# Performance work log

Measured on AMD Instinct MI355X. Metric: run time of the kernel, lower is better.

## Reference

```python
import jax, jax.numpy as jnp
import numpy as np

GAMMA = 5e-4
IN_DIM, HID = 512, 4096
N = HID  # batch must equal hidden_dim for classifier(gram) to type-check


def setup_inputs() -> dict:
    key = jax.random.key(0)
    ks = jax.random.split(key, 7)
    s = lambda fan_in: 1.0 / np.sqrt(fan_in)
    return {
        "x": jax.random.normal(ks[0], (N, IN_DIM), jnp.float32),
        "W1": jax.random.uniform(ks[1], (HID, IN_DIM), jnp.float32, -s(IN_DIM), s(IN_DIM)),
        "b1": jax.random.uniform(ks[2], (HID,), jnp.float32, -s(IN_DIM), s(IN_DIM)),
        "W2": jax.random.uniform(ks[3], (HID, HID), jnp.float32, -s(HID), s(HID)),
        "b2": jax.random.uniform(ks[4], (HID,), jnp.float32, -s(HID), s(HID)),
        "Wc": jax.random.uniform(ks[5], (1, HID), jnp.float32, -s(HID), s(HID)),
        "bc": jax.random.uniform(ks[6], (1,), jnp.float32, -s(HID), s(HID)),
    }


def reference(x, W1, b1, W2, b2, Wc, bc):
    h = jnp.tanh(x @ W1.T + b1)          # [N, HID]
    h = jnp.tanh(h @ W2.T + b2)          # [N, HID]
    # KernelLayer: support = h.detach() (first call), RBF gram via cdist+exp
    support = jax.lax.stop_gradient(h)   # [N, HID]
    sq = (jnp.sum(h * h, axis=1, keepdims=True)
          + jnp.sum(support * support, axis=1)[None, :]
          - 2.0 * (h @ support.T))       # [N, N] squared distances
    gram = jnp.exp(-GAMMA * sq)
    return gram @ Wc.T + bc              # [N, 1]
```

## Files before the change

### kernel.cpp

```cpp
#include <hip/hip_runtime.h>
#include <hip/hip_bf16.h>


#define NROWS 4096
#define HID   4096
#define INDIM 512
#define GAMMA_F 5e-4f

typedef float f32x4  __attribute__((ext_vector_type(4)));
typedef int   i32x4  __attribute__((ext_vector_type(4)));
typedef int   i32x8  __attribute__((ext_vector_type(8)));

#define BAR() asm volatile("s_barrier" ::: "memory")
#define SCALE1 0x7F7F7F7F

__device__ __forceinline__ unsigned short f2bf_rne(float f) {
  union { float f; unsigned int u; } v; v.f = f;
  unsigned int r = v.u + 0x7FFFu + ((v.u >> 16) & 1u);
  return (unsigned short)(r >> 16);
}

__device__ __forceinline__ unsigned char f2e4m3(float x) {
  unsigned int u = __float_as_uint(x);
  unsigned char s = (unsigned char)((u >> 24) & 0x80u);
  float a = fabsf(x);
  if (a >= 448.f) return s | 0x7E;
  if (a < 0.015625f) {
    int q = (int)rintf(a * 512.f);
    return s | (unsigned char)q;
  }
  unsigned int ua = u & 0x7fffffffu;
  ua += 0x7FFFFu + ((ua >> 20) & 1u);
  int e = (int)(ua >> 23) - 127;
  unsigned int m = (ua >> 20) & 7u;
  return s | (unsigned char)(((e + 7) << 3) | m);
}

__global__ void cast_f32_fp8(const float* __restrict__ src,
                             unsigned char* __restrict__ dst,
                             float scale, int n8) {
  int i = blockIdx.x * blockDim.x + threadIdx.x;
  if (i >= n8) return;
  const float4* s = (const float4*)src;
  float4 v0 = s[i * 2], v1 = s[i * 2 + 1];
  unsigned int r0 = (unsigned int)f2e4m3(v0.x * scale)
                  | ((unsigned int)f2e4m3(v0.y * scale) << 8)
                  | ((unsigned int)f2e4m3(v0.z * scale) << 16)
                  | ((unsigned int)f2e4m3(v0.w * scale) << 24);
  unsigned int r1 = (unsigned int)f2e4m3(v1.x * scale)
                  | ((unsigned int)f2e4m3(v1.y * scale) << 8)
                  | ((unsigned int)f2e4m3(v1.z * scale) << 16)
                  | ((unsigned int)f2e4m3(v1.w * scale) << 24);
  uint2 o; o.x = r0; o.y = r1;
  ((uint2*)dst)[i] = o;
}

__global__ void init_vecs(float* __restrict__ out, float* __restrict__ norms,
                          const float* __restrict__ bc, int n) {
  int i = blockIdx.x * blockDim.x + threadIdx.x;
  if (i < n) { out[i] = bc[0]; norms[i] = 0.f; }
}

__device__ __forceinline__ void gload16(const void* g, void* l) {
  __builtin_amdgcn_global_load_lds(
      (const __attribute__((address_space(1))) void*)g,
      (__attribute__((address_space(3))) void*)l, 16, 0, 0);
}

template <int EPI>
__global__ __launch_bounds__(512, 2)
void gemm256_fp8(const unsigned char* __restrict__ A, const unsigned char* __restrict__ B,
                 int K, int N,
                 const float* __restrict__ bias, unsigned char* __restrict__ Hout,
                 float* __restrict__ norms_out) {
  __shared__ __align__(16) unsigned char As[2][2][256 * 64];
  __shared__ __align__(16) unsigned char Bs[2][2][256 * 64];

  const int tid  = threadIdx.x;
  const int lane = tid & 63;
  const int wave = tid >> 6;
  const int wr = wave >> 2, wc = wave & 3;
  const int fr = lane & 15, fq = lane >> 4;

  const int nwg = gridDim.x;
  const int cpx = nwg >> 3;
  const int bid = blockIdx.x;
  const int swzb = (bid & 7) * cpx + (bid >> 3);
  const int nbx = N >> 8;
  const int brow = (swzb / nbx) << 8;
  const int bcol = (swzb % nbx) << 8;

  const unsigned char* ap[4]; const unsigned char* bp[4]; int ldq[4];
#pragma unroll
  for (int q = 0; q < 4; ++q) {
    int idx = q * 512 + tid;
    int h   = idx >> 10;
    int row = (idx >> 2) & 255;
    int c   = idx & 3;
    int gcol = ((((c ^ ((row >> 1) & 3)) << 1) | h) << 4);
    ap[q] = A + (size_t)(brow + row) * K + gcol;
    bp[q] = B + (size_t)(bcol + row) * K + gcol;
    ldq[q] = (q * 512 + wave * 64) * 16;
  }
#define STAGE_A(p, tt) do { int kk = (tt) * 128;              \
    gload16(ap[0] + kk, &As[p][0][0] + ldq[0]);               \
    gload16(ap[1] + kk, &As[p][0][0] + ldq[1]);               \
    gload16(ap[2] + kk, &As[p][0][0] + ldq[2]);               \
    gload16(ap[3] + kk, &As[p][0][0] + ldq[3]); } while (0)
#define STAGE_B(p, tt) do { int kk = (tt) * 128;              \
    gload16(bp[0] + kk, &Bs[p][0][0] + ldq[0]);               \
    gload16(bp[1] + kk, &Bs[p][0][0] + ldq[1]);               \
    gload16(bp[2] + kk, &Bs[p][0][0] + ldq[2]);               \
    gload16(bp[3] + kk, &Bs[p][0][0] + ldq[3]); } while (0)

  int aoff[8], boff[4];
#pragma unroll
  for (int mi = 0; mi < 8; ++mi) {
    int row = wr * 128 + mi * 16 + fr;
    aoff[mi] = row * 64 + ((fq ^ ((row >> 1) & 3)) << 4);
  }
#pragma unroll
  for (int nj = 0; nj < 4; ++nj) {
    int row = wc * 64 + nj * 16 + fr;
    boff[nj] = row * 64 + ((fq ^ ((row >> 1) & 3)) << 4);
  }

#define LDFRAG(dst, base0, off) do {                                \
    i32x4 lo_ = *(const i32x4*)((base0) + (off));                   \
    i32x4 hi_ = *(const i32x4*)((base0) + 16384 + (off));           \
    dst[0]=lo_[0]; dst[1]=lo_[1]; dst[2]=lo_[2]; dst[3]=lo_[3];     \
    dst[4]=hi_[0]; dst[5]=hi_[1]; dst[6]=hi_[2]; dst[7]=hi_[3]; } while (0)

#define MFMA16(d, a, b) \
    d = __builtin_amdgcn_mfma_scale_f32_16x16x128_f8f6f4( \
        a, b, d, 0, 0, 0, SCALE1, 0, SCALE1)

  const int NT = K >> 7;

  STAGE_A(0, 0); STAGE_B(0, 0);
  STAGE_A(1, 1); STAGE_B(1, 1);
  asm volatile("s_waitcnt vmcnt(8)" ::: "memory");
  BAR();

  f32x4 acc[8][4] = {};
  i32x8 afr[4], bfr[4];

  for (int t = 0; t < NT; ++t) {
    const int p = t & 1;
    int t2 = t + 2; if (t2 >= NT) t2 -= NT;

#pragma unroll
    for (int mi = 0; mi < 4; ++mi) LDFRAG(afr[mi], &As[p][0][0], aoff[mi]);
#pragma unroll
    for (int nj = 0; nj < 4; ++nj) LDFRAG(bfr[nj], &Bs[p][0][0], boff[nj]);
    asm volatile("s_waitcnt lgkmcnt(0)" ::: "memory");
    BAR();
    STAGE_B(p, t2);
    __builtin_amdgcn_sched_barrier(0);
    __builtin_amdgcn_s_setprio(1);
#pragma unroll
    for (int mi = 0; mi < 4; ++mi)
#pragma unroll
      for (int nj = 0; nj < 4; ++nj) MFMA16(acc[mi][nj], afr[mi], bfr[nj]);
    __builtin_amdgcn_s_setprio(0);

#pragma unroll
    for (int mi = 0; mi < 4; ++mi) LDFRAG(afr[mi], &As[p][0][0], aoff[4 + mi]);
    asm volatile("s_waitcnt lgkmcnt(0)" ::: "memory");
    BAR();
    STAGE_A(p, t2);
    __builtin_amdgcn_sched_barrier(0);
    __builtin_amdgcn_s_setprio(1);
#pragma unroll
    for (int mi = 0; mi < 4; ++mi)
#pragma unroll
      for (int nj = 0; nj < 4; ++nj) MFMA16(acc[4 + mi][nj], afr[mi], bfr[nj]);
    __builtin_amdgcn_s_setprio(0);
    asm volatile("s_waitcnt vmcnt(8)" ::: "memory");
    BAR();
  }
  asm volatile("s_waitcnt vmcnt(0)" ::: "memory");

  const float rescale = (EPI == 0) ? (1.f / 512.f) : (1.f / 1024.f);
  float bv[4];
#pragma unroll
  for (int nj = 0; nj < 4; ++nj) bv[nj] = bias[bcol + wc * 64 + nj * 16 + fr];
#pragma unroll
  for (int mi = 0; mi < 8; ++mi) {
    int row0 = brow + wr * 128 + mi * 16 + fq * 4;
#pragma unroll
    for (int rr = 0; rr < 4; ++rr) {
      float ns = 0.f;
#pragma unroll
      for (int nj = 0; nj < 4; ++nj) {
        int col = bcol + wc * 64 + nj * 16 + fr;
        float v = tanhf(acc[mi][nj][rr] * rescale + bv[nj]);
        Hout[(size_t)(row0 + rr) * N + col] = f2e4m3(8.f * v);
        if (EPI == 2) ns += v * v;
      }
      if (EPI == 2) {
        ns += __shfl_xor(ns, 1);
        ns += __shfl_xor(ns, 2);
        ns += __shfl_xor(ns, 4);
        ns += __shfl_xor(ns, 8);
        if (fr == 0) atomicAdd(&norms_out[row0 + rr], ns);
      }
    }
  }
#undef STAGE_A
#undef STAGE_B
#undef LDFRAG
#undef MFMA16
}

__global__ __launch_bounds__(256, 2)
void gram_tri(const unsigned char* __restrict__ H, int K,
              const float* __restrict__ norms, const float* __restrict__ Wc,
              float* __restrict__ out) {
  __shared__ __align__(16) unsigned char As[2][128 * 64];
  __shared__ __align__(16) unsigned char Bs[2][128 * 64];

  const int tid  = threadIdx.x;
  const int lane = tid & 63;
  const int wave = tid >> 6;
  const int wr = wave >> 1, wc = wave & 1;
  const int fr = lane & 15, fq = lane >> 4;

  const int bid = blockIdx.x;
  const int swzb = (bid & 7) * 66 + (bid >> 3);
  int I = (int)((sqrtf(8.0f * (float)swzb + 1.0f) - 1.0f) * 0.5f);
  while ((I + 1) * (I + 2) / 2 <= swzb) ++I;
  while (I * (I + 1) / 2 > swzb) --I;
  const int J = swzb - I * (I + 1) / 2;
  const int brow = I << 7, bcol = J << 7;
  const bool diag = (I == J);

  const unsigned char* ap[4]; const unsigned char* bp[4]; int ldq[4];
#pragma unroll
  for (int q = 0; q < 4; ++q) {
    int idx = q * 256 + tid;
    int h   = idx >> 9;
    int row = (idx >> 2) & 127;
    int c   = idx & 3;
    int gcol = ((((c ^ ((row >> 1) & 3)) << 1) | h) << 4);
    ap[q] = H + (size_t)(brow + row) * K + gcol;
    bp[q] = H + (size_t)(bcol + row) * K + gcol;
    ldq[q] = (q * 256 + wave * 64) * 16;
  }

  int aoff[4], boff[4];
#pragma unroll
  for (int mi = 0; mi < 4; ++mi) {
    int row = wr * 64 + mi * 16 + fr;
    aoff[mi] = row * 64 + ((fq ^ ((row >> 1) & 3)) << 4);
  }
#pragma unroll
  for (int nj = 0; nj < 4; ++nj) {
    int row = wc * 64 + nj * 16 + fr;
    boff[nj] = row * 64 + ((fq ^ ((row >> 1) & 3)) << 4);
  }

#define LDFRAG(dst, base0, off) do {                                \
    i32x4 lo_ = *(const i32x4*)((base0) + (off));                   \
    i32x4 hi_ = *(const i32x4*)((base0) + 8192 + (off));            \
    dst[0]=lo_[0]; dst[1]=lo_[1]; dst[2]=lo_[2]; dst[3]=lo_[3];     \
    dst[4]=hi_[0]; dst[5]=hi_[1]; dst[6]=hi_[2]; dst[7]=hi_[3]; } while (0)

  f32x4 acc[4][4] = {};

  for (int t = 0; t < (K >> 7); ++t) {
    __syncthreads();
    {
      int kk = t * 128;
      gload16(ap[0] + kk, &As[0][0] + ldq[0]);
      gload16(ap[1] + kk, &As[0][0] + ldq[1]);
      gload16(ap[2] + kk, &As[0][0] + ldq[2]);
      gload16(ap[3] + kk, &As[0][0] + ldq[3]);
      gload16(bp[0] + kk, &Bs[0][0] + ldq[0]);
      gload16(bp[1] + kk, &Bs[0][0] + ldq[1]);
      gload16(bp[2] + kk, &Bs[0][0] + ldq[2]);
      gload16(bp[3] + kk, &Bs[0][0] + ldq[3]);
    }
    __syncthreads();

    i32x8 af[4], bf[4];
#pragma unroll
    for (int mi = 0; mi < 4; ++mi) LDFRAG(af[mi], &As[0][0], aoff[mi]);
#pragma unroll
    for (int nj = 0; nj < 4; ++nj) LDFRAG(bf[nj], &Bs[0][0], boff[nj]);
#pragma unroll
    for (int mi = 0; mi < 4; ++mi)
#pragma unroll
      for (int nj = 0; nj < 4; ++nj)
        acc[mi][nj] = __builtin_amdgcn_mfma_scale_f32_16x16x128_f8f6f4(
            af[mi], bf[nj], acc[mi][nj], 0, 0, 0, SCALE1, 0, SCALE1);
  }
#undef LDFRAG

  float ncol[4], wcv[4];
#pragma unroll
  for (int nj = 0; nj < 4; ++nj) {
    int col = bcol + wc * 64 + nj * 16 + fr;
    ncol[nj] = norms[col];
    wcv[nj]  = Wc[col];
  }
  float colpart[4] = {0.f, 0.f, 0.f, 0.f};
#pragma unroll
  for (int mi = 0; mi < 4; ++mi) {
    int row0 = brow + wr * 64 + mi * 16 + fq * 4;
    float4 nr4  = *(const float4*)&norms[row0];
    float4 wcr4 = *(const float4*)&Wc[row0];
#pragma unroll
    for (int rr = 0; rr < 4; ++rr) {
      float nrow = (rr == 0) ? nr4.x : (rr == 1) ? nr4.y : (rr == 2) ? nr4.z : nr4.w;
      float wrow = (rr == 0) ? wcr4.x : (rr == 1) ? wcr4.y : (rr == 2) ? wcr4.z : wcr4.w;
      float rowpart = 0.f;
#pragma unroll
      for (int nj = 0; nj < 4; ++nj) {
        float sq = nrow + ncol[nj] - acc[mi][nj][rr] * 0.03125f;
        float e = __expf(-GAMMA_F * sq);
        rowpart += e * wcv[nj];
        colpart[nj] += e * wrow;
      }
      rowpart += __shfl_xor(rowpart, 1);
      rowpart += __shfl_xor(rowpart, 2);
      rowpart += __shfl_xor(rowpart, 4);
      rowpart += __shfl_xor(rowpart, 8);
      if (fr == 0) atomicAdd(&out[row0 + rr], rowpart);
    }
  }
  if (!diag) {
#pragma unroll
    for (int nj = 0; nj < 4; ++nj) {
      colpart[nj] += __shfl_xor(colpart[nj], 16);
      colpart[nj] += __shfl_xor(colpart[nj], 32);
      if (fq == 0) atomicAdd(&out[bcol + wc * 64 + nj * 16 + fr], colpart[nj]);
    }
  }
}

extern "C" void kernel_launch(void* const* d_in, const int* in_sizes, int n_in,
                              void* d_out, int out_size, void* d_ws, size_t ws_size,
                              hipStream_t stream) {
  const float* x  = (const float*)d_in[0];
  const float* W1 = (const float*)d_in[1];
  const float* b1 = (const float*)d_in[2];
  const float* W2 = (const float*)d_in[3];
  const float* b2 = (const float*)d_in[4];
  const float* Wc = (const float*)d_in[5];
  const float* bc = (const float*)d_in[6];
  float* out = (float*)d_out;

  char* ws = (char*)d_ws;
  unsigned char* xq  = (unsigned char*)ws; ws += (size_t)NROWS * INDIM;
  unsigned char* w1q = (unsigned char*)ws; ws += (size_t)HID * INDIM;
  unsigned char* w2q = (unsigned char*)ws; ws += (size_t)HID * HID;
  unsigned char* h1q = (unsigned char*)ws; ws += (size_t)NROWS * HID;
  unsigned char* h2q = (unsigned char*)ws; ws += (size_t)NROWS * HID;
  float* norms = (float*)ws;                ws += (size_t)NROWS * 4;

  {
    int n8 = NROWS * INDIM / 8;
    cast_f32_fp8<<<(n8 + 255) / 256, 256, 0, stream>>>(x, xq, 16.f, n8);
    cast_f32_fp8<<<(n8 + 255) / 256, 256, 0, stream>>>(W1, w1q, 32.f, n8);
    int m8 = HID * HID / 8;
    cast_f32_fp8<<<(m8 + 255) / 256, 256, 0, stream>>>(W2, w2q, 128.f, m8);
  }

  const int grid = (NROWS / 256) * (HID / 256);

  gemm256_fp8<0><<<grid, 512, 0, stream>>>(xq, w1q, INDIM, HID, b1, h1q, nullptr);
  init_vecs<<<(NROWS + 255) / 256, 256, 0, stream>>>(out, norms, bc, NROWS);
  gemm256_fp8<2><<<grid, 512, 0, stream>>>(h1q, w2q, HID, HID, b2, h2q, norms);
  gram_tri<<<528, 256, 0, stream>>>(h2q, HID, norms, Wc, out);
}
```

Measured before the change: 201.1 us.

## Double-buffer gram kernel loads and fuse cast/init kernels into one prep launch

The gram_tri kernel moves from a single LDS buffer with two syncthreads per K-step to a double-buffered pipeline that prefetches two tiles ahead, overlapping global-to-LDS loads with MFMA work. The three cast kernels and the init kernel are merged into one grid-stride prep kernel to cut launch overhead. The fragment load now uses a shufflevector, and the prefetch index clamps to the last tile instead of wrapping around. The extra LDS buffers double gram_tri's shared memory, which may reduce occupancy.

```diff
diff --git a/kernel.cpp b/kernel.cpp
--- a/kernel.cpp
+++ b/kernel.cpp
@@ -13,12 +13,6 @@
 
 #define BAR() asm volatile("s_barrier" ::: "memory")
 #define SCALE1 0x7F7F7F7F
-
-__device__ __forceinline__ unsigned short f2bf_rne(float f) {
-  union { float f; unsigned int u; } v; v.f = f;
-  unsigned int r = v.u + 0x7FFFu + ((v.u >> 16) & 1u);
-  return (unsigned short)(r >> 16);
-}
 
 __device__ __forceinline__ unsigned char f2e4m3(float x) {
   unsigned int u = __float_as_uint(x);
@@ -36,29 +30,35 @@
   return s | (unsigned char)(((e + 7) << 3) | m);
 }
 
-__global__ void cast_f32_fp8(const float* __restrict__ src,
-                             unsigned char* __restrict__ dst,
-                             float scale, int n8) {
-  int i = blockIdx.x * blockDim.x + threadIdx.x;
-  if (i >= n8) return;
-  const float4* s = (const float4*)src;
-  float4 v0 = s[i * 2], v1 = s[i * 2 + 1];
-  unsigned int r0 = (unsigned int)f2e4m3(v0.x * scale)
-                  | ((unsigned int)f2e4m3(v0.y * scale) << 8)
-                  | ((unsigned int)f2e4m3(v0.z * scale) << 16)
-                  | ((unsigned int)f2e4m3(v0.w * scale) << 24);
-  unsigned int r1 = (unsigned int)f2e4m3(v1.x * scale)
-                  | ((unsigned int)f2e4m3(v1.y * scale) << 8)
-                  | ((unsigned int)f2e4m3(v1.z * scale) << 16)
-                  | ((unsigned int)f2e4m3(v1.w * scale) << 24);
-  uint2 o; o.x = r0; o.y = r1;
-  ((uint2*)dst)[i] = o;
-}
-
-__global__ void init_vecs(float* __restrict__ out, float* __restrict__ norms,
-                          const float* __restrict__ bc, int n) {
-  int i = blockIdx.x * blockDim.x + threadIdx.x;
-  if (i < n) { out[i] = bc[0]; norms[i] = 0.f; }
+__global__ void prep(const float* __restrict__ x, const float* __restrict__ W1,
+                     const float* __restrict__ W2, const float* __restrict__ bc,
+                     unsigned char* __restrict__ xq, unsigned char* __restrict__ w1q,
+                     unsigned char* __restrict__ w2q,
+                     float* __restrict__ out, float* __restrict__ norms) {
+  const int gi = blockIdx.x * blockDim.x + threadIdx.x;
+  if (gi < NROWS) { out[gi] = bc[0]; norms[gi] = 0.f; }
+  const int NX  = NROWS * INDIM / 8;
+  const int NW2 = HID * HID / 8;
+  const int total = 2 * NX + NW2;
+  const int stride = gridDim.x * blockDim.x;
+  for (int i = gi; i < total; i += stride) {
+    const float* src; unsigned char* dst; float sc; int j;
+    if (i < NX)            { src = x;  dst = xq;  sc = 16.f;  j = i; }
+    else if (i < 2 * NX)   { src = W1; dst = w1q; sc = 32.f;  j = i - NX; }
+    else                   { src = W2; dst = w2q; sc = 128.f; j = i - 2 * NX; }
+    float4 v0 = ((const float4*)src)[j * 2];
+    float4 v1 = ((const float4*)src)[j * 2 + 1];
+    unsigned int r0 = (unsigned int)f2e4m3(v0.x * sc)
+                    | ((unsigned int)f2e4m3(v0.y * sc) << 8)
+                    | ((unsigned int)f2e4m3(v0.z * sc) << 16)
+                    | ((unsigned int)f2e4m3(v0.w * sc) << 24);
+    unsigned int r1 = (unsigned int)f2e4m3(v1.x * sc)
+                    | ((unsigned int)f2e4m3(v1.y * sc) << 8)
+                    | ((unsigned int)f2e4m3(v1.z * sc) << 16)
+                    | ((unsigned int)f2e4m3(v1.w * sc) << 24);
+    uint2 o; o.x = r0; o.y = r1;
+    ((uint2*)dst)[j] = o;
+  }
 }
 
 __device__ __forceinline__ void gload16(const void* g, void* l) {
@@ -66,6 +66,15 @@
       (const __attribute__((address_space(1))) void*)g,
       (__attribute__((address_space(3))) void*)l, 16, 0, 0);
 }
+
+#define LDFRAG(dst, base0, off, RSTRIDE) do {                       \
+    i32x4 lo_ = *(const i32x4*)((base0) + (off));                   \
+    i32x4 hi_ = *(const i32x4*)((base0) + (RSTRIDE) + (off));       \
+    dst = __builtin_shufflevector(lo_, hi_, 0, 1, 2, 3, 4, 5, 6, 7); } while (0)
+
+#define MFMA16(d, a, b) \
+    d = __builtin_amdgcn_mfma_scale_f32_16x16x128_f8f6f4( \
+        a, b, d, 0, 0, 0, SCALE1, 0, SCALE1)
 
 template <int EPI>
 __global__ __launch_bounds__(512, 2)
@@ -125,16 +134,6 @@
     boff[nj] = row * 64 + ((fq ^ ((row >> 1) & 3)) << 4);
   }
 
-#define LDFRAG(dst, base0, off) do {                                \
-    i32x4 lo_ = *(const i32x4*)((base0) + (off));                   \
-    i32x4 hi_ = *(const i32x4*)((base0) + 16384 + (off));           \
-    dst[0]=lo_[0]; dst[1]=lo_[1]; dst[2]=lo_[2]; dst[3]=lo_[3];     \
-    dst[4]=hi_[0]; dst[5]=hi_[1]; dst[6]=hi_[2]; dst[7]=hi_[3]; } while (0)
-
-#define MFMA16(d, a, b) \
-    d = __builtin_amdgcn_mfma_scale_f32_16x16x128_f8f6f4( \
-        a, b, d, 0, 0, 0, SCALE1, 0, SCALE1)
-
   const int NT = K >> 7;
 
   STAGE_A(0, 0); STAGE_B(0, 0);
@@ -147,12 +146,12 @@
 
   for (int t = 0; t < NT; ++t) {
     const int p = t & 1;
-    int t2 = t + 2; if (t2 >= NT) t2 -= NT;
-
-#pragma unroll
-    for (int mi = 0; mi < 4; ++mi) LDFRAG(afr[mi], &As[p][0][0], aoff[mi]);
-#pragma unroll
-    for (int nj = 0; nj < 4; ++nj) LDFRAG(bfr[nj], &Bs[p][0][0], boff[nj]);
+    int t2 = t + 2; if (t2 >= NT) t2 = NT - 1;
+
+#pragma unroll
+    for (int mi = 0; mi < 4; ++mi) LDFRAG(afr[mi], &As[p][0][0], aoff[mi], 16384);
+#pragma unroll
+    for (int nj = 0; nj < 4; ++nj) LDFRAG(bfr[nj], &Bs[p][0][0], boff[nj], 16384);
     asm volatile("s_waitcnt lgkmcnt(0)" ::: "memory");
     BAR();
     STAGE_B(p, t2);
@@ -165,7 +164,7 @@
     __builtin_amdgcn_s_setprio(0);
 
 #pragma unroll
-    for (int mi = 0; mi < 4; ++mi) LDFRAG(afr[mi], &As[p][0][0], aoff[4 + mi]);
+    for (int mi = 0; mi < 4; ++mi) LDFRAG(afr[mi], &As[p][0][0], aoff[4 + mi], 16384);
     asm volatile("s_waitcnt lgkmcnt(0)" ::: "memory");
     BAR();
     STAGE_A(p, t2);
@@ -209,16 +208,14 @@
   }
 #undef STAGE_A
 #undef STAGE_B
-#undef LDFRAG
-#undef MFMA16
 }
 
 __global__ __launch_bounds__(256, 2)
 void gram_tri(const unsigned char* __restrict__ H, int K,
               const float* __restrict__ norms, const float* __restrict__ Wc,
               float* __restrict__ out) {
-  __shared__ __align__(16) unsigned char As[2][128 * 64];
-  __shared__ __align__(16) unsigned char Bs[2][128 * 64];
+  __shared__ __align__(16) unsigned char As[2][2][128 * 64];
+  __shared__ __align__(16) unsigned char Bs[2][2][128 * 64];
 
   const int tid  = threadIdx.x;
   const int lane = tid & 63;
@@ -247,6 +244,16 @@
     bp[q] = H + (size_t)(bcol + row) * K + gcol;
     ldq[q] = (q * 256 + wave * 64) * 16;
   }
+#define GSTAGE_A(p, tt) do { int kk = (tt) * 128;             \
+    gload16(ap[0] + kk, &As[p][0][0] + ldq[0]);               \
+    gload16(ap[1] + kk, &As[p][0][0] + ldq[1]);               \
+    gload16(ap[2] + kk, &As[p][0][0] + ldq[2]);               \
+    gload16(ap[3] + kk, &As[p][0][0] + ldq[3]); } while (0)
+#define GSTAGE_B(p, tt) do { int kk = (tt) * 128;             \
+    gload16(bp[0] + kk, &Bs[p][0][0] + ldq[0]);               \
+    gload16(bp[1] + kk, &Bs[p][0][0] + ldq[1]);               \
+    gload16(bp[2] + kk, &Bs[p][0][0] + ldq[2]);               \
+    gload16(bp[3] + kk, &Bs[p][0][0] + ldq[3]); } while (0)
 
   int aoff[4], boff[4];
 #pragma unroll
@@ -260,42 +267,38 @@
     boff[nj] = row * 64 + ((fq ^ ((row >> 1) & 3)) << 4);
   }
 
-#define LDFRAG(dst, base0, off) do {                                \
-    i32x4 lo_ = *(const i32x4*)((base0) + (off));                   \
-    i32x4 hi_ = *(const i32x4*)((base0) + 8192 + (off));            \
-    dst[0]=lo_[0]; dst[1]=lo_[1]; dst[2]=lo_[2]; dst[3]=lo_[3];     \
-    dst[4]=hi_[0]; dst[5]=hi_[1]; dst[6]=hi_[2]; dst[7]=hi_[3]; } while (0)
+  const int NT = K >> 7;
+
+  GSTAGE_A(0, 0); GSTAGE_B(0, 0);
+  GSTAGE_A(1, 1); GSTAGE_B(1, 1);
+  asm volatile("s_waitcnt vmcnt(8)" ::: "memory");
+  BAR();
 
   f32x4 acc[4][4] = {};
 
-  for (int t = 0; t < (K >> 7); ++t) {
-    __syncthreads();
-    {
-      int kk = t * 128;
-      gload16(ap[0] + kk, &As[0][0] + ldq[0]);
-      gload16(ap[1] + kk, &As[0][0] + ldq[1]);
-      gload16(ap[2] + kk, &As[0][0] + ldq[2]);
-      gload16(ap[3] + kk, &As[0][0] + ldq[3]);
-      gload16(bp[0] + kk, &Bs[0][0] + ldq[0]);
-      gload16(bp[1] + kk, &Bs[0][0] + ldq[1]);
-      gload16(bp[2] + kk, &Bs[0][0] + ldq[2]);
-      gload16(bp[3] + kk, &Bs[0][0] + ldq[3]);
-    }
-    __syncthreads();
+  for (int t = 0; t < NT; ++t) {
+    const int p = t & 1;
+    int t2 = t + 2; if (t2 >= NT) t2 = NT - 1;
 
     i32x8 af[4], bf[4];
 #pragma unroll
-    for (int mi = 0; mi < 4; ++mi) LDFRAG(af[mi], &As[0][0], aoff[mi]);
-#pragma unroll
-    for (int nj = 0; nj < 4; ++nj) LDFRAG(bf[nj], &Bs[0][0], boff[nj]);
+    for (int mi = 0; mi < 4; ++mi) LDFRAG(af[mi], &As[p][0][0], aoff[mi], 8192);
+#pragma unroll
+    for (int nj = 0; nj < 4; ++nj) LDFRAG(bf[nj], &Bs[p][0][0], boff[nj], 8192);
+    asm volatile("s_waitcnt lgkmcnt(0)" ::: "memory");
+    BAR();
+    GSTAGE_A(p, t2); GSTAGE_B(p, t2);
+    __builtin_amdgcn_sched_barrier(0);
+    __builtin_amdgcn_s_setprio(1);
 #pragma unroll
     for (int mi = 0; mi < 4; ++mi)
 #pragma unroll
-      for (int nj = 0; nj < 4; ++nj)
-        acc[mi][nj] = __builtin_amdgcn_mfma_scale_f32_16x16x128_f8f6f4(
-            af[mi], bf[nj], acc[mi][nj], 0, 0, 0, SCALE1, 0, SCALE1);
-  }
-#undef LDFRAG
+      for (int nj = 0; nj < 4; ++nj) MFMA16(acc[mi][nj], af[mi], bf[nj]);
+    __builtin_amdgcn_s_setprio(0);
+    asm volatile("s_waitcnt vmcnt(8)" ::: "memory");
+    BAR();
+  }
+  asm volatile("s_waitcnt vmcnt(0)" ::: "memory");
 
   float ncol[4], wcv[4];
 #pragma unroll
@@ -337,6 +340,8 @@
       if (fq == 0) atomicAdd(&out[bcol + wc * 64 + nj * 16 + fr], colpart[nj]);
     }
   }
+#undef GSTAGE_A
+#undef GSTAGE_B
 }
 
 extern "C" void kernel_launch(void* const* d_in, const int* in_sizes, int n_in,
@@ -359,18 +364,11 @@
   unsigned char* h2q = (unsigned char*)ws; ws += (size_t)NROWS * HID;
   float* norms = (float*)ws;                ws += (size_t)NROWS * 4;
 
-  {
-    int n8 = NROWS * INDIM / 8;
-    cast_f32_fp8<<<(n8 + 255) / 256, 256, 0, stream>>>(x, xq, 16.f, n8);
-    cast_f32_fp8<<<(n8 + 255) / 256, 256, 0, stream>>>(W1, w1q, 32.f, n8);
-    int m8 = HID * HID / 8;
-    cast_f32_fp8<<<(m8 + 255) / 256, 256, 0, stream>>>(W2, w2q, 128.f, m8);
-  }
+  prep<<<2048, 256, 0, stream>>>(x, W1, W2, bc, xq, w1q, w2q, out, norms);
 
   const int grid = (NROWS / 256) * (HID / 256);
 
   gemm256_fp8<0><<<grid, 512, 0, stream>>>(xq, w1q, INDIM, HID, b1, h1q, nullptr);
-  init_vecs<<<(NROWS + 255) / 256, 256, 0, stream>>>(out, norms, bc, NROWS);
   gemm256_fp8<2><<<grid, 512, 0, stream>>>(h1q, w2q, HID, HID, b2, h2q, norms);
   gram_tri<<<528, 256, 0, stream>>>(h2q, HID, norms, Wc, out);
 }
```

Result: slower. 209.2 us (+4.0%).
